# Optimization experiments

Measured on AMD Instinct MI355X. Metric: run time of the kernel, lower is better.

Reference implementation:

```python
import jax, jax.numpy as jnp
import numpy as np

N = 12288      # nodes
E = 393216     # edges (avg degree 32)
D_IN = 512
D_H = 256      # interm_dim
D_Z = 64       # latent_dim


def setup_inputs() -> dict:
    key = jax.random.key(0)
    ks = jax.random.split(key, 9)
    X = jax.random.normal(ks[0], (N, D_IN), jnp.float32)
    edge_index = jax.random.randint(ks[1], (2, E), 0, N, dtype=jnp.int64)
    # GCNConv weights (glorot-ish scaling)
    W1 = jax.random.normal(ks[2], (D_IN, D_H), jnp.float32) / np.sqrt(D_IN)
    b1 = jnp.zeros((D_H,), jnp.float32)
    Wmu = jax.random.normal(ks[3], (D_H, D_Z), jnp.float32) / np.sqrt(D_H)
    bmu = jnp.zeros((D_Z,), jnp.float32)
    Wsig = jax.random.normal(ks[4], (D_H, 1), jnp.float32) / np.sqrt(D_H)
    bsig = jnp.zeros((1,), jnp.float32)
    # reparameterization noise (torch: Normal(0,1).sample(mus.size()))
    eps = jax.random.normal(ks[5], (N, D_Z), jnp.float32)
    return {"X": X, "edge_index": edge_index, "W1": W1, "b1": b1,
            "Wmu": Wmu, "bmu": bmu, "Wsig": Wsig, "bsig": bsig, "eps": eps}


def _gcn_conv(h_in, W, b, src, dst, norm):
    # GCNConv: linear transform then symmetric-normalized aggregation with self-loops
    h = h_in @ W + b                                   # [N, F_out]
    msg = h[src] * norm[src, None]                     # gather + scale
    agg = jax.ops.segment_sum(msg, dst, num_segments=N)
    # self-loop contribution: norm_i * norm_i * h_i
    return norm[:, None] * (agg + norm[:, None] * h)


def reference(X, edge_index, W1, b1, Wmu, bmu, Wsig, bsig, eps):
    src, dst = edge_index[0], edge_index[1]
    # degree of A + I (edge weight 1, plus self loop)
    deg = jax.ops.segment_sum(jnp.ones((E,), X.dtype), dst, num_segments=N) + 1.0
    norm = jax.lax.rsqrt(deg)                          # D^{-1/2}

    # encoder
    H = jax.nn.relu(_gcn_conv(X, W1, b1, src, dst, norm))   # [N, D_H]; dropout p=0.0
    mus = _gcn_conv(H, Wmu, bmu, src, dst, norm)            # [N, D_Z]
    logsigma2s = _gcn_conv(H, Wsig, bsig, src, dst, norm)   # [N, 1]

    # reparameterize
    sigmas = jnp.exp(0.5 * logsigma2s)                      # [N, 1]
    Z = mus + sigmas * eps                                  # [N, D_Z]

    # dense decoder
    ZZt = Z @ Z.T                                           # [N, N]
    return ZZt, mus, logsigma2s
```

## Files before the change

### kernel.cpp

```cpp
#include <hip/hip_runtime.h>

#define N_NODES 12288
#define N_EDGES 393216
#define DIN 512
#define DH 256
#define DZ 64

typedef __bf16 bf16x8 __attribute__((ext_vector_type(8)));
typedef float f32x4 __attribute__((ext_vector_type(4)));
typedef unsigned short u16x8 __attribute__((ext_vector_type(8)));

static __device__ __forceinline__ unsigned short f2bf(float f) {
    unsigned int u = __float_as_uint(f);
    unsigned int r = (u + 0x7fffu + ((u >> 16) & 1u)) >> 16;
    return (unsigned short)r;
}
static __device__ __forceinline__ float bf2f(unsigned short u) {
    return __uint_as_float((unsigned int)u << 16);
}

__global__ __launch_bounds__(256) void k_prep(const float* __restrict__ X, unsigned short* __restrict__ Xb,
                                              const float* __restrict__ W1, unsigned short* __restrict__ W1T,
                                              const float* __restrict__ Wmu, unsigned short* __restrict__ WmuT,
                                              const int* __restrict__ dst, int* __restrict__ deg) {
    int b = blockIdx.x;
    if (b < 6144) {
        int i = b * 256 + threadIdx.x;
        float4 v = ((const float4*)X)[i];
        ushort4 o;
        o.x = f2bf(v.x); o.y = f2bf(v.y); o.z = f2bf(v.z); o.w = f2bf(v.w);
        ((ushort4*)Xb)[i] = o;
    } else if (b < 6656) {
        int i = (b - 6144) * 256 + threadIdx.x;
        int c = i >> 9, k = i & 511;
        W1T[i] = f2bf(W1[k * DH + c]);
    } else if (b < 6720) {
        int i = (b - 6656) * 256 + threadIdx.x;
        int c = i >> 8, k = i & 255;
        WmuT[i] = f2bf(Wmu[k * DZ + c]);
    } else {
        int e = (b - 6720) * 256 + threadIdx.x;
        atomicAdd(&deg[dst[e]], 1);
    }
}

__global__ __launch_bounds__(1024) void k_scan(const int* __restrict__ cnt, int* __restrict__ rp,
                                               float* __restrict__ norm) {
    __shared__ int sp[1024];
    int t = threadIdx.x;
    int base = t * 12;
    int loc[12];
    int s = 0;
#pragma unroll
    for (int j = 0; j < 12; ++j) {
        int c = cnt[base + j];
        norm[base + j] = rsqrtf((float)c + 1.0f);
        loc[j] = s; s += c;
    }
    sp[t] = s;
    __syncthreads();
    for (int off = 1; off < 1024; off <<= 1) {
        int v = (t >= off) ? sp[t - off] : 0;
        __syncthreads();
        sp[t] += v;
        __syncthreads();
    }
    int pre = (t == 0) ? 0 : sp[t - 1];
#pragma unroll
    for (int j = 0; j < 12; ++j) rp[base + j] = pre + loc[j];
    if (t == 1023) rp[N_NODES] = sp[1023];
}

__global__ __launch_bounds__(256) void k_scatter(const int* __restrict__ src, const int* __restrict__ dst,
                                                 const int* __restrict__ rp, int* __restrict__ cursor,
                                                 int* __restrict__ ssrc) {
    int e = blockIdx.x * 256 + threadIdx.x;
    int d = dst[e];
    int pos = atomicAdd(&cursor[d], 1);
    ssrc[rp[d] + pos] = src[e];
}

__global__ __launch_bounds__(512) void k_gemm1(const unsigned short* __restrict__ Xb,
                                               const unsigned short* __restrict__ W1T,
                                               const float* __restrict__ b1, const float* __restrict__ norm,
                                               unsigned short* __restrict__ g1) {
    int wid = threadIdx.x >> 6;
    int lane = threadIdx.x & 63;
    int ln = lane & 15, kg = lane >> 4;
    int rb = blockIdx.x * 256 + (wid >> 1) * 64;
    int cb = blockIdx.y * 128 + (wid & 1) * 64;
    f32x4 acc[4][4] = {};
    const unsigned short* xa = Xb + (size_t)(rb + ln) * DIN + kg * 8;
    const unsigned short* wb = W1T + (size_t)(cb + ln) * DIN + kg * 8;
    for (int ks = 0; ks < 16; ++ks) {
        int k0 = ks * 32;
        bf16x8 a[4], b[4];
#pragma unroll
        for (int m = 0; m < 4; ++m) a[m] = *(const bf16x8*)(xa + (size_t)m * 16 * DIN + k0);
#pragma unroll
        for (int n = 0; n < 4; ++n) b[n] = *(const bf16x8*)(wb + (size_t)n * 16 * DIN + k0);
#pragma unroll
        for (int m = 0; m < 4; ++m)
#pragma unroll
            for (int n = 0; n < 4; ++n)
                acc[m][n] = __builtin_amdgcn_mfma_f32_16x16x32_bf16(a[m], b[n], acc[m][n], 0, 0, 0);
    }
#pragma unroll
    for (int m = 0; m < 4; ++m)
#pragma unroll
        for (int r = 0; r < 4; ++r) {
            int row = rb + m * 16 + kg * 4 + r;
            float ni = norm[row];
#pragma unroll
            for (int n = 0; n < 4; ++n) {
                int col = cb + n * 16 + ln;
                g1[(size_t)row * DH + col] = f2bf(ni * (acc[m][n][r] + b1[col]));
            }
        }
}

__global__ __launch_bounds__(256) void k_agg1(const unsigned short* __restrict__ g1,
                                              const int* __restrict__ rp, const int* __restrict__ ssrc,
                                              const float* __restrict__ norm, const float* __restrict__ Wsig,
                                              unsigned short* __restrict__ G2, float* __restrict__ tvec,
                                              float* __restrict__ qv) {
    int w = threadIdx.x >> 6;
    int lane = threadIdx.x & 63;
    int half = lane >> 5, lh = lane & 31;
    int i = blockIdx.x * 4 + w;
    int beg = rp[i], end = rp[i + 1];
    int cnt = end - beg;
    int itn = (cnt + 1) >> 1;
    size_t cho = (size_t)lh * 8;
    float a8[8] = {};
    float ssum = 0.f;
#pragma unroll 2
    for (int it = 0; it < itn; ++it) {
        int e = beg + it * 2 + half;
        if (e < end) {
            int s = ssrc[e];
            u16x8 v = *(const u16x8*)(g1 + ((size_t)s << 8) + cho);
            ssum += norm[s];
#pragma unroll
            for (int j = 0; j < 8; ++j) a8[j] += bf2f(v[j]);
        }
    }
    if (half == 0) {
        u16x8 v = *(const u16x8*)(g1 + ((size_t)i << 8) + cho);
#pragma unroll
        for (int j = 0; j < 8; ++j) a8[j] += bf2f(v[j]);
    }
#pragma unroll
    for (int j = 0; j < 8; ++j) a8[j] += __shfl_xor(a8[j], 32);
    ssum += __shfl_xor(ssum, 32);
    float ni = norm[i];
    const float4 ws0 = *(const float4*)(Wsig + cho);
    const float4 ws1 = *(const float4*)(Wsig + cho + 4);
    float g[8];
#pragma unroll
    for (int j = 0; j < 8; ++j) g[j] = ni * fmaxf(ni * a8[j], 0.f);
    float qp = g[0] * ws0.x + g[1] * ws0.y + g[2] * ws0.z + g[3] * ws0.w
             + g[4] * ws1.x + g[5] * ws1.y + g[6] * ws1.z + g[7] * ws1.w;
    if (half == 0) {
        u16x8 o;
#pragma unroll
        for (int j = 0; j < 8; ++j) o[j] = f2bf(g[j]);
        *(u16x8*)(G2 + ((size_t)i << 8) + cho) = o;
    }
#pragma unroll
    for (int m = 16; m >= 1; m >>= 1) qp += __shfl_xor(qp, m);
    if (lane == 0) {
        tvec[i] = ssum + ni;
        qv[i] = qp;
    }
}

__global__ __launch_bounds__(256) void k_gemm2(const unsigned short* __restrict__ G2,
                                               const unsigned short* __restrict__ WmuT,
                                               unsigned short* __restrict__ Pb) {
    int wid = threadIdx.x >> 6;
    int lane = threadIdx.x & 63;
    int ln = lane & 15, kg = lane >> 4;
    int rb = blockIdx.x * 128 + wid * 32;
    f32x4 acc[2][4] = {};
    const unsigned short* xa = G2 + (size_t)(rb + ln) * DH + kg * 8;
    const unsigned short* wb = WmuT + (size_t)ln * DH + kg * 8;
    for (int ks = 0; ks < 8; ++ks) {
        int k0 = ks * 32;
        bf16x8 a[2], b[4];
#pragma unroll
        for (int m = 0; m < 2; ++m) a[m] = *(const bf16x8*)(xa + (size_t)m * 16 * DH + k0);
#pragma unroll
        for (int n = 0; n < 4; ++n) b[n] = *(const bf16x8*)(wb + (size_t)n * 16 * DH + k0);
#pragma unroll
        for (int m = 0; m < 2; ++m)
#pragma unroll
            for (int n = 0; n < 4; ++n)
                acc[m][n] = __builtin_amdgcn_mfma_f32_16x16x32_bf16(a[m], b[n], acc[m][n], 0, 0, 0);
    }
#pragma unroll
    for (int m = 0; m < 2; ++m)
#pragma unroll
        for (int n = 0; n < 4; ++n)
#pragma unroll
            for (int r = 0; r < 4; ++r) {
                int row = rb + m * 16 + kg * 4 + r;
                int col = n * 16 + ln;
                Pb[(size_t)row * DZ + col] = f2bf(acc[m][n][r]);
            }
}

__global__ __launch_bounds__(256) void k_agg2(const unsigned short* __restrict__ Pb,
                                              const float* __restrict__ qv,
                                              const int* __restrict__ rp, const int* __restrict__ ssrc,
                                              const float* __restrict__ norm, const float* __restrict__ tvec,
                                              const float* __restrict__ bmu, const float* __restrict__ bsig,
                                              const float* __restrict__ eps,
                                              float* __restrict__ mus_out, float* __restrict__ logs_out,
                                              unsigned short* __restrict__ Zb) {
    int w = threadIdx.x >> 6;
    int lane = threadIdx.x & 63;
    int grp = lane >> 4, li = lane & 15;
    int i = blockIdx.x * 4 + w;
    int beg = rp[i], end = rp[i + 1];
    int cnt = end - beg;
    int itn = (cnt + 3) >> 2;
    int co = li * 4;
    float a4[4] = {};
    float qa = 0.f;
#pragma unroll 2
    for (int it = 0; it < itn; ++it) {
        int e = beg + it * 4 + grp;
        if (e < end) {
            int s = ssrc[e];
            ushort4 v = *(const ushort4*)(Pb + ((size_t)s << 6) + co);
            qa += qv[s];
            a4[0] += bf2f(v.x); a4[1] += bf2f(v.y); a4[2] += bf2f(v.z); a4[3] += bf2f(v.w);
        }
    }
    if (grp == 0) {
        ushort4 v = *(const ushort4*)(Pb + ((size_t)i << 6) + co);
        qa += qv[i];
        a4[0] += bf2f(v.x); a4[1] += bf2f(v.y); a4[2] += bf2f(v.z); a4[3] += bf2f(v.w);
    }
#pragma unroll
    for (int j = 0; j < 4; ++j) {
        a4[j] += __shfl_xor(a4[j], 16);
        a4[j] += __shfl_xor(a4[j], 32);
    }
    qa += __shfl_xor(qa, 16);
    qa += __shfl_xor(qa, 32);
    float ni = norm[i], tv = tvec[i];
    float ls = ni * (qa + bsig[0] * tv);
    float sig = expf(0.5f * ls);
    if (lane == 0) logs_out[i] = ls;
    if (lane < 16) {
        const float4 bm = *(const float4*)(bmu + co);
        float4 mu;
        mu.x = ni * (a4[0] + bm.x * tv);
        mu.y = ni * (a4[1] + bm.y * tv);
        mu.z = ni * (a4[2] + bm.z * tv);
        mu.w = ni * (a4[3] + bm.w * tv);
        size_t oidx = ((size_t)i << 6) + co;
        *(float4*)(mus_out + oidx) = mu;
        const float4 ep = *(const float4*)(eps + oidx);
        ushort4 z;
        z.x = f2bf(mu.x + sig * ep.x);
        z.y = f2bf(mu.y + sig * ep.y);
        z.z = f2bf(mu.z + sig * ep.z);
        z.w = f2bf(mu.w + sig * ep.w);
        *(ushort4*)(Zb + oidx) = z;
    }
}

#define LPAD 260
__global__ __launch_bounds__(256) void k_zzt(const unsigned short* __restrict__ Zb, float* __restrict__ out) {
    __shared__ float lds[32 * LPAD];
    int w = threadIdx.x >> 6;
    int lane = threadIdx.x & 63;
    int ln = lane & 15, kg = lane >> 4;
    int rb = blockIdx.x * 64;
    int cb = blockIdx.y * 256 + w * 64;
    bf16x8 a[4][2], b[4][2];
#pragma unroll
    for (int m = 0; m < 4; ++m)
#pragma unroll
        for (int kc = 0; kc < 2; ++kc)
            a[m][kc] = *(const bf16x8*)(Zb + (size_t)(rb + m * 16 + ln) * DZ + kc * 32 + kg * 8);
#pragma unroll
    for (int n = 0; n < 4; ++n)
#pragma unroll
        for (int kc = 0; kc < 2; ++kc)
            b[n][kc] = *(const bf16x8*)(Zb + (size_t)(cb + n * 16 + ln) * DZ + kc * 32 + kg * 8);
    f32x4 acc[4][4] = {};
#pragma unroll
    for (int m = 0; m < 4; ++m)
#pragma unroll
        for (int n = 0; n < 4; ++n) {
            acc[m][n] = __builtin_amdgcn_mfma_f32_16x16x32_bf16(a[m][0], b[n][0], acc[m][n], 0, 0, 0);
            acc[m][n] = __builtin_amdgcn_mfma_f32_16x16x32_bf16(a[m][1], b[n][1], acc[m][n], 0, 0, 0);
        }
    int c4 = (threadIdx.x & 63) * 4;
    int rw = threadIdx.x >> 6;
    size_t colbase = (size_t)blockIdx.y * 256 + c4;
#pragma unroll
    for (int p = 0; p < 2; ++p) {
        if (p) __syncthreads();
#pragma unroll
        for (int mm = 0; mm < 2; ++mm) {
            int m = p * 2 + mm;
#pragma unroll
            for (int n = 0; n < 4; ++n)
#pragma unroll
                for (int r = 0; r < 4; ++r)
                    lds[(mm * 16 + kg * 4 + r) * LPAD + w * 64 + n * 16 + ln] = acc[m][n][r];
        }
        __syncthreads();
#pragma unroll
        for (int it = 0; it < 8; ++it) {
            int rl = it * 4 + rw;
            f32x4 v = *(const f32x4*)&lds[rl * LPAD + c4];
            __builtin_nontemporal_store(v, (f32x4*)(out + (size_t)(rb + p * 32 + rl) * N_NODES + colbase));
        }
    }
}

extern "C" void kernel_launch(void* const* d_in, const int* in_sizes, int n_in,
                              void* d_out, int out_size, void* d_ws, size_t ws_size,
                              hipStream_t stream) {
    const float* X = (const float*)d_in[0];
    const int* edge = (const int*)d_in[1];
    const float* W1 = (const float*)d_in[2];
    const float* b1 = (const float*)d_in[3];
    const float* Wmu = (const float*)d_in[4];
    const float* bmu = (const float*)d_in[5];
    const float* Wsig = (const float*)d_in[6];
    const float* bsig = (const float*)d_in[7];
    const float* eps = (const float*)d_in[8];

    const int* esrc = edge;
    const int* edst = edge + N_EDGES;

    char* w = (char*)d_ws;
    int* deg = (int*)w;            w += (size_t)N_NODES * 4;
    int* cursor = (int*)w;         w += (size_t)N_NODES * 4;
    float* norm = (float*)w;       w += (size_t)N_NODES * 4;
    float* tvec = (float*)w;       w += (size_t)N_NODES * 4;
    float* qv = (float*)w;         w += (size_t)N_NODES * 4;
    int* rowptr = (int*)w;         w += (size_t)(N_NODES + 64) * 4;
    int* ssrc = (int*)w;           w += (size_t)N_EDGES * 4;
    unsigned short* Xb = (unsigned short*)w;   w += (size_t)N_NODES * DIN * 2;
    unsigned short* W1T = (unsigned short*)w;  w += (size_t)DIN * DH * 2;
    unsigned short* WmuT = (unsigned short*)w; w += (size_t)DH * DZ * 2;
    unsigned short* g1 = (unsigned short*)w;   w += (size_t)N_NODES * DH * 2;
    unsigned short* G2 = (unsigned short*)w;   w += (size_t)N_NODES * DH * 2;
    unsigned short* Pb = (unsigned short*)w;   w += (size_t)N_NODES * DZ * 2;
    unsigned short* Zb = (unsigned short*)w;   w += (size_t)N_NODES * DZ * 2;

    float* out_zzt = (float*)d_out;
    float* out_mus = out_zzt + (size_t)N_NODES * N_NODES;
    float* out_logs = out_mus + (size_t)N_NODES * DZ;

    hipMemsetAsync(d_ws, 0, (size_t)N_NODES * 8, stream);
    k_prep<<<8256, 256, 0, stream>>>(X, Xb, W1, W1T, Wmu, WmuT, edst, deg);
    k_scan<<<1, 1024, 0, stream>>>(deg, rowptr, norm);
    k_scatter<<<N_EDGES / 256, 256, 0, stream>>>(esrc, edst, rowptr, cursor, ssrc);
    k_gemm1<<<dim3(N_NODES / 256, 2), 512, 0, stream>>>(Xb, W1T, b1, norm, g1);
    k_agg1<<<N_NODES / 4, 256, 0, stream>>>(g1, rowptr, ssrc, norm, Wsig, G2, tvec, qv);
    k_gemm2<<<N_NODES / 128, 256, 0, stream>>>(G2, WmuT, Pb);
    k_agg2<<<N_NODES / 4, 256, 0, stream>>>(Pb, qv, rowptr, ssrc, norm, tvec, bmu, bsig, eps,
                                            out_mus, out_logs, Zb);
    k_zzt<<<dim3(N_NODES / 64, N_NODES / 256), 256, 0, stream>>>(Zb, out_zzt);
}
```

Baseline: 278.4 us.

## Split hidden features into halves, XCD-aware aggregation, fold Wsig into gemm2

Stores the hidden activations as two 128-column halves and maps aggregation blocks so that each group of XCDs gathers only one half. The goal is a smaller gathered working set per L2. The Wsig projection moves out of agg1 and becomes an extra MFMA column tile in gemm2 (WmuT80), and cursor zeroing moves into the scan kernel so the memset shrinks. The ZZt kernel also swaps its grid axes and drops nontemporal stores. The trade-offs are twice as many agg1 blocks with duplicated index and rowptr reads, a different write-back pattern for the large ZZt output, and reliance on the assumed round-robin block-to-XCD mapping.

```diff
diff --git a/kernel.cpp b/kernel.cpp
--- a/kernel.cpp
+++ b/kernel.cpp
@@ -5,10 +5,11 @@
 #define DIN 512
 #define DH 256
 #define DZ 64
+#define HALF 128
 
 typedef __bf16 bf16x8 __attribute__((ext_vector_type(8)));
 typedef float f32x4 __attribute__((ext_vector_type(4)));
-typedef unsigned short u16x8 __attribute__((ext_vector_type(8)));
+typedef unsigned short u16x4 __attribute__((ext_vector_type(4)));
 
 static __device__ __forceinline__ unsigned short f2bf(float f) {
     unsigned int u = __float_as_uint(f);
@@ -21,7 +22,8 @@
 
 __global__ __launch_bounds__(256) void k_prep(const float* __restrict__ X, unsigned short* __restrict__ Xb,
                                               const float* __restrict__ W1, unsigned short* __restrict__ W1T,
-                                              const float* __restrict__ Wmu, unsigned short* __restrict__ WmuT,
+                                              const float* __restrict__ Wmu, const float* __restrict__ Wsig,
+                                              unsigned short* __restrict__ WmuT80,
                                               const int* __restrict__ dst, int* __restrict__ deg) {
     int b = blockIdx.x;
     if (b < 6144) {
@@ -34,18 +36,19 @@
         int i = (b - 6144) * 256 + threadIdx.x;
         int c = i >> 9, k = i & 511;
         W1T[i] = f2bf(W1[k * DH + c]);
-    } else if (b < 6720) {
+    } else if (b < 6736) {
         int i = (b - 6656) * 256 + threadIdx.x;
         int c = i >> 8, k = i & 255;
-        WmuT[i] = f2bf(Wmu[k * DZ + c]);
+        float v = (c < 64) ? Wmu[k * DZ + c] : ((c == 64) ? Wsig[k] : 0.f);
+        WmuT80[i] = f2bf(v);
     } else {
-        int e = (b - 6720) * 256 + threadIdx.x;
+        int e = (b - 6736) * 256 + threadIdx.x;
         atomicAdd(&deg[dst[e]], 1);
     }
 }
 
 __global__ __launch_bounds__(1024) void k_scan(const int* __restrict__ cnt, int* __restrict__ rp,
-                                               float* __restrict__ norm) {
+                                               float* __restrict__ norm, int* __restrict__ cursor) {
     __shared__ int sp[1024];
     int t = threadIdx.x;
     int base = t * 12;
@@ -55,6 +58,7 @@
     for (int j = 0; j < 12; ++j) {
         int c = cnt[base + j];
         norm[base + j] = rsqrtf((float)c + 1.0f);
+        cursor[base + j] = 0;
         loc[j] = s; s += c;
     }
     sp[t] = s;
@@ -83,7 +87,7 @@
 __global__ __launch_bounds__(512) void k_gemm1(const unsigned short* __restrict__ Xb,
                                                const unsigned short* __restrict__ W1T,
                                                const float* __restrict__ b1, const float* __restrict__ norm,
-                                               unsigned short* __restrict__ g1) {
+                                               unsigned short* __restrict__ g1a, unsigned short* __restrict__ g1b) {
     int wid = threadIdx.x >> 6;
     int lane = threadIdx.x & 63;
     int ln = lane & 15, kg = lane >> 4;
@@ -105,6 +109,8 @@
             for (int n = 0; n < 4; ++n)
                 acc[m][n] = __builtin_amdgcn_mfma_f32_16x16x32_bf16(a[m], b[n], acc[m][n], 0, 0, 0);
     }
+    unsigned short* gout = (cb < 128) ? g1a : g1b;
+    int cbh = cb & 64;
 #pragma unroll
     for (int m = 0; m < 4; ++m)
 #pragma unroll
@@ -114,100 +120,97 @@
 #pragma unroll
             for (int n = 0; n < 4; ++n) {
                 int col = cb + n * 16 + ln;
-                g1[(size_t)row * DH + col] = f2bf(ni * (acc[m][n][r] + b1[col]));
+                gout[(size_t)row * HALF + cbh + n * 16 + ln] = f2bf(ni * (acc[m][n][r] + b1[col]));
             }
         }
 }
 
-__global__ __launch_bounds__(256) void k_agg1(const unsigned short* __restrict__ g1,
+__global__ __launch_bounds__(256) void k_agg1(const unsigned short* __restrict__ g1a,
+                                              const unsigned short* __restrict__ g1b,
                                               const int* __restrict__ rp, const int* __restrict__ ssrc,
-                                              const float* __restrict__ norm, const float* __restrict__ Wsig,
-                                              unsigned short* __restrict__ G2, float* __restrict__ tvec,
-                                              float* __restrict__ qv) {
+                                              const float* __restrict__ norm,
+                                              unsigned short* __restrict__ G2a, unsigned short* __restrict__ G2b,
+                                              float* __restrict__ tvec) {
+    int b = blockIdx.x;
+    int xcdp = b & 7;
+    int pass = xcdp >> 2;
+    int sub = xcdp & 3;
+    int idx = (b >> 3) * 4 + sub;
     int w = threadIdx.x >> 6;
     int lane = threadIdx.x & 63;
     int half = lane >> 5, lh = lane & 31;
-    int i = blockIdx.x * 4 + w;
+    int i = idx * 4 + w;
     int beg = rp[i], end = rp[i + 1];
     int cnt = end - beg;
     int itn = (cnt + 1) >> 1;
-    size_t cho = (size_t)lh * 8;
-    float a8[8] = {};
+    int cho = lh * 4;
+    const unsigned short* gsrc = pass ? g1b : g1a;
+    float a4[4] = {};
     float ssum = 0.f;
 #pragma unroll 2
     for (int it = 0; it < itn; ++it) {
         int e = beg + it * 2 + half;
         if (e < end) {
-            int s = ssrc[e];
-            u16x8 v = *(const u16x8*)(g1 + ((size_t)s << 8) + cho);
-            ssum += norm[s];
-#pragma unroll
-            for (int j = 0; j < 8; ++j) a8[j] += bf2f(v[j]);
+            int s = __builtin_nontemporal_load(ssrc + e);
+            ushort4 v = *(const ushort4*)(gsrc + (size_t)s * HALF + cho);
+            if (pass == 0) ssum += norm[s];
+            a4[0] += bf2f(v.x); a4[1] += bf2f(v.y); a4[2] += bf2f(v.z); a4[3] += bf2f(v.w);
         }
     }
     if (half == 0) {
-        u16x8 v = *(const u16x8*)(g1 + ((size_t)i << 8) + cho);
-#pragma unroll
-        for (int j = 0; j < 8; ++j) a8[j] += bf2f(v[j]);
-    }
-#pragma unroll
-    for (int j = 0; j < 8; ++j) a8[j] += __shfl_xor(a8[j], 32);
+        ushort4 v = *(const ushort4*)(gsrc + (size_t)i * HALF + cho);
+        a4[0] += bf2f(v.x); a4[1] += bf2f(v.y); a4[2] += bf2f(v.z); a4[3] += bf2f(v.w);
+    }
+#pragma unroll
+    for (int j = 0; j < 4; ++j) a4[j] += __shfl_xor(a4[j], 32);
     ssum += __shfl_xor(ssum, 32);
     float ni = norm[i];
-    const float4 ws0 = *(const float4*)(Wsig + cho);
-    const float4 ws1 = *(const float4*)(Wsig + cho + 4);
-    float g[8];
-#pragma unroll
-    for (int j = 0; j < 8; ++j) g[j] = ni * fmaxf(ni * a8[j], 0.f);
-    float qp = g[0] * ws0.x + g[1] * ws0.y + g[2] * ws0.z + g[3] * ws0.w
-             + g[4] * ws1.x + g[5] * ws1.y + g[6] * ws1.z + g[7] * ws1.w;
     if (half == 0) {
-        u16x8 o;
-#pragma unroll
-        for (int j = 0; j < 8; ++j) o[j] = f2bf(g[j]);
-        *(u16x8*)(G2 + ((size_t)i << 8) + cho) = o;
-    }
-#pragma unroll
-    for (int m = 16; m >= 1; m >>= 1) qp += __shfl_xor(qp, m);
-    if (lane == 0) {
-        tvec[i] = ssum + ni;
-        qv[i] = qp;
-    }
-}
-
-__global__ __launch_bounds__(256) void k_gemm2(const unsigned short* __restrict__ G2,
-                                               const unsigned short* __restrict__ WmuT,
-                                               unsigned short* __restrict__ Pb) {
+        u16x4 o;
+        o[0] = f2bf(ni * fmaxf(ni * a4[0], 0.f));
+        o[1] = f2bf(ni * fmaxf(ni * a4[1], 0.f));
+        o[2] = f2bf(ni * fmaxf(ni * a4[2], 0.f));
+        o[3] = f2bf(ni * fmaxf(ni * a4[3], 0.f));
+        unsigned short* gdst = pass ? G2b : G2a;
+        __builtin_nontemporal_store(o, (u16x4*)(gdst + (size_t)i * HALF + cho));
+    }
+    if (pass == 0 && lane == 0) tvec[i] = ssum + ni;
+}
+
+__global__ __launch_bounds__(256) void k_gemm2(const unsigned short* __restrict__ G2a,
+                                               const unsigned short* __restrict__ G2b,
+                                               const unsigned short* __restrict__ WmuT80,
+                                               unsigned short* __restrict__ Pb, float* __restrict__ qv) {
     int wid = threadIdx.x >> 6;
     int lane = threadIdx.x & 63;
     int ln = lane & 15, kg = lane >> 4;
     int rb = blockIdx.x * 128 + wid * 32;
-    f32x4 acc[2][4] = {};
-    const unsigned short* xa = G2 + (size_t)(rb + ln) * DH + kg * 8;
-    const unsigned short* wb = WmuT + (size_t)ln * DH + kg * 8;
+    f32x4 acc[2][5] = {};
+    const unsigned short* wb = WmuT80 + (size_t)ln * 256 + kg * 8;
     for (int ks = 0; ks < 8; ++ks) {
         int k0 = ks * 32;
-        bf16x8 a[2], b[4];
-#pragma unroll
-        for (int m = 0; m < 2; ++m) a[m] = *(const bf16x8*)(xa + (size_t)m * 16 * DH + k0);
-#pragma unroll
-        for (int n = 0; n < 4; ++n) b[n] = *(const bf16x8*)(wb + (size_t)n * 16 * DH + k0);
+        const unsigned short* xsrc = (ks < 4) ? (G2a + kg * 8 + ks * 32) : (G2b + kg * 8 + (ks - 4) * 32);
+        bf16x8 a[2], b[5];
+#pragma unroll
+        for (int m = 0; m < 2; ++m) a[m] = *(const bf16x8*)(xsrc + (size_t)(rb + m * 16 + ln) * HALF);
+#pragma unroll
+        for (int n = 0; n < 5; ++n) b[n] = *(const bf16x8*)(wb + (size_t)n * 16 * 256 + k0);
 #pragma unroll
         for (int m = 0; m < 2; ++m)
 #pragma unroll
+            for (int n = 0; n < 5; ++n)
+                acc[m][n] = __builtin_amdgcn_mfma_f32_16x16x32_bf16(a[m], b[n], acc[m][n], 0, 0, 0);
+    }
+#pragma unroll
+    for (int m = 0; m < 2; ++m)
+#pragma unroll
+        for (int r = 0; r < 4; ++r) {
+            int row = rb + m * 16 + kg * 4 + r;
+#pragma unroll
             for (int n = 0; n < 4; ++n)
-                acc[m][n] = __builtin_amdgcn_mfma_f32_16x16x32_bf16(a[m], b[n], acc[m][n], 0, 0, 0);
-    }
-#pragma unroll
-    for (int m = 0; m < 2; ++m)
-#pragma unroll
-        for (int n = 0; n < 4; ++n)
-#pragma unroll
-            for (int r = 0; r < 4; ++r) {
-                int row = rb + m * 16 + kg * 4 + r;
-                int col = n * 16 + ln;
-                Pb[(size_t)row * DZ + col] = f2bf(acc[m][n][r]);
-            }
+                Pb[(size_t)row * DZ + n * 16 + ln] = f2bf(acc[m][n][r]);
+            if (ln == 0) qv[row] = acc[m][4][r];
+        }
 }
 
 __global__ __launch_bounds__(256) void k_agg2(const unsigned short* __restrict__ Pb,
@@ -279,8 +282,8 @@
     int w = threadIdx.x >> 6;
     int lane = threadIdx.x & 63;
     int ln = lane & 15, kg = lane >> 4;
-    int rb = blockIdx.x * 64;
-    int cb = blockIdx.y * 256 + w * 64;
+    int rb = blockIdx.y * 64;
+    int cb = blockIdx.x * 256 + w * 64;
     bf16x8 a[4][2], b[4][2];
 #pragma unroll
     for (int m = 0; m < 4; ++m)
@@ -302,7 +305,7 @@
         }
     int c4 = (threadIdx.x & 63) * 4;
     int rw = threadIdx.x >> 6;
-    size_t colbase = (size_t)blockIdx.y * 256 + c4;
+    size_t colbase = (size_t)blockIdx.x * 256 + c4;
 #pragma unroll
     for (int p = 0; p < 2; ++p) {
         if (p) __syncthreads();
@@ -320,7 +323,7 @@
         for (int it = 0; it < 8; ++it) {
             int rl = it * 4 + rw;
             f32x4 v = *(const f32x4*)&lds[rl * LPAD + c4];
-            __builtin_nontemporal_store(v, (f32x4*)(out + (size_t)(rb + p * 32 + rl) * N_NODES + colbase));
+            *(f32x4*)(out + (size_t)(rb + p * 32 + rl) * N_NODES + colbase) = v;
         }
     }
 }
@@ -349,26 +352,28 @@
     float* qv = (float*)w;         w += (size_t)N_NODES * 4;
     int* rowptr = (int*)w;         w += (size_t)(N_NODES + 64) * 4;
     int* ssrc = (int*)w;           w += (size_t)N_EDGES * 4;
-    unsigned short* Xb = (unsigned short*)w;   w += (size_t)N_NODES * DIN * 2;
-    unsigned short* W1T = (unsigned short*)w;  w += (size_t)DIN * DH * 2;
-    unsigned short* WmuT = (unsigned short*)w; w += (size_t)DH * DZ * 2;
-    unsigned short* g1 = (unsigned short*)w;   w += (size_t)N_NODES * DH * 2;
-    unsigned short* G2 = (unsigned short*)w;   w += (size_t)N_NODES * DH * 2;
-    unsigned short* Pb = (unsigned short*)w;   w += (size_t)N_NODES * DZ * 2;
-    unsigned short* Zb = (unsigned short*)w;   w += (size_t)N_NODES * DZ * 2;
+    unsigned short* Xb = (unsigned short*)w;    w += (size_t)N_NODES * DIN * 2;
+    unsigned short* W1T = (unsigned short*)w;   w += (size_t)DIN * DH * 2;
+    unsigned short* WmuT80 = (unsigned short*)w; w += (size_t)80 * 256 * 2;
+    unsigned short* g1a = (unsigned short*)w;   w += (size_t)N_NODES * HALF * 2;
+    unsigned short* g1b = (unsigned short*)w;   w += (size_t)N_NODES * HALF * 2;
+    unsigned short* G2a = (unsigned short*)w;   w += (size_t)N_NODES * HALF * 2;
+    unsigned short* G2b = (unsigned short*)w;   w += (size_t)N_NODES * HALF * 2;
+    unsigned short* Pb = (unsigned short*)w;    w += (size_t)N_NODES * DZ * 2;
+    unsigned short* Zb = (unsigned short*)w;    w += (size_t)N_NODES * DZ * 2;
 
     float* out_zzt = (float*)d_out;
     float* out_mus = out_zzt + (size_t)N_NODES * N_NODES;
     float* out_logs = out_mus + (size_t)N_NODES * DZ;
 
-    hipMemsetAsync(d_ws, 0, (size_t)N_NODES * 8, stream);
-    k_prep<<<8256, 256, 0, stream>>>(X, Xb, W1, W1T, Wmu, WmuT, edst, deg);
-    k_scan<<<1, 1024, 0, stream>>>(deg, rowptr, norm);
+    (void)hipMemsetAsync(deg, 0, (size_t)N_NODES * 4, stream);
+    k_prep<<<8272, 256, 0, stream>>>(X, Xb, W1, W1T, Wmu, Wsig, WmuT80, edst, deg);
+    k_scan<<<1, 1024, 0, stream>>>(deg, rowptr, norm, cursor);
     k_scatter<<<N_EDGES / 256, 256, 0, stream>>>(esrc, edst, rowptr, cursor, ssrc);
-    k_gemm1<<<dim3(N_NODES / 256, 2), 512, 0, stream>>>(Xb, W1T, b1, norm, g1);
-    k_agg1<<<N_NODES / 4, 256, 0, stream>>>(g1, rowptr, ssrc, norm, Wsig, G2, tvec, qv);
-    k_gemm2<<<N_NODES / 128, 256, 0, stream>>>(G2, WmuT, Pb);
+    k_gemm1<<<dim3(N_NODES / 256, 2), 512, 0, stream>>>(Xb, W1T, b1, norm, g1a, g1b);
+    k_agg1<<<N_NODES / 2, 256, 0, stream>>>(g1a, g1b, rowptr, ssrc, norm, G2a, G2b, tvec);
+    k_gemm2<<<N_NODES / 128, 256, 0, stream>>>(G2a, G2b, WmuT80, Pb, qv);
     k_agg2<<<N_NODES / 4, 256, 0, stream>>>(Pb, qv, rowptr, ssrc, norm, tvec, bmu, bsig, eps,
                                             out_mus, out_logs, Zb);
-    k_zzt<<<dim3(N_NODES / 64, N_NODES / 256), 256, 0, stream>>>(Zb, out_zzt);
-}
+    k_zzt<<<dim3(N_NODES / 256, N_NODES / 64), 256, 0, stream>>>(Zb, out_zzt);
+}
```

Result: slower. 285.3 us (+2.5%).

## Fuse all pre-decoder stages into one persistent kernel with grid barriers

Applied to the files above, without the earlier changes.

Replaces the seven separate launches (prep, scan, scatter, gemm1, agg1, gemm2, agg2) with one persistent kernel of 512 blocks. The stages are separated by software grid barriers built from atomic counters. This removes per-launch overhead and the tail gaps between the many small kernels. The costs are less parallelism in each stage: gemm1 uses smaller tiles with fewer waves, and the scan now runs on a single block. The design also depends on all 512 blocks being resident at once, otherwise the barriers deadlock.

```diff
diff --git a/kernel.cpp b/kernel.cpp
--- a/kernel.cpp
+++ b/kernel.cpp
@@ -5,6 +5,8 @@
 #define DIN 512
 #define DH 256
 #define DZ 64
+#define NB 512
+#define NT 256
 
 typedef __bf16 bf16x8 __attribute__((ext_vector_type(8)));
 typedef float f32x4 __attribute__((ext_vector_type(4)));
@@ -19,257 +21,256 @@
     return __uint_as_float((unsigned int)u << 16);
 }
 
-__global__ __launch_bounds__(256) void k_prep(const float* __restrict__ X, unsigned short* __restrict__ Xb,
-                                              const float* __restrict__ W1, unsigned short* __restrict__ W1T,
-                                              const float* __restrict__ Wmu, unsigned short* __restrict__ WmuT,
-                                              const int* __restrict__ dst, int* __restrict__ deg) {
-    int b = blockIdx.x;
-    if (b < 6144) {
-        int i = b * 256 + threadIdx.x;
+static __device__ __forceinline__ void gridbar(int* bar, int p) {
+    __syncthreads();
+    if (threadIdx.x == 0) {
+        __threadfence();
+        __hip_atomic_fetch_add(&bar[p], 1, __ATOMIC_RELEASE, __HIP_MEMORY_SCOPE_AGENT);
+        while (__hip_atomic_load(&bar[p], __ATOMIC_ACQUIRE, __HIP_MEMORY_SCOPE_AGENT) < NB)
+            __builtin_amdgcn_s_sleep(2);
+        __threadfence();
+    }
+    __syncthreads();
+}
+
+__global__ __launch_bounds__(256, 2) void k_mega(
+    const float* __restrict__ X, const int* __restrict__ esrc, const int* __restrict__ edst,
+    const float* __restrict__ W1, const float* __restrict__ Wmu, const float* __restrict__ Wsig,
+    const float* __restrict__ b1, const float* __restrict__ bmu, const float* __restrict__ bsig,
+    const float* __restrict__ eps,
+    int* __restrict__ bar, int* __restrict__ deg, int* __restrict__ cursor,
+    float* __restrict__ norm, float* __restrict__ tvec, float* __restrict__ qv,
+    int* __restrict__ rp, int* __restrict__ ssrc,
+    unsigned short* __restrict__ Xb, unsigned short* __restrict__ W1T, unsigned short* __restrict__ WmuT,
+    unsigned short* __restrict__ g1, unsigned short* __restrict__ G2, unsigned short* __restrict__ Pb,
+    float* __restrict__ mus_out, float* __restrict__ logs_out, unsigned short* __restrict__ Zb) {
+
+    __shared__ int sp[256];
+    const int tid = threadIdx.x;
+    const int bid = blockIdx.x;
+    const int gtid = bid * NT + tid;
+    const int w = tid >> 6, lane = tid & 63;
+    const int gw = bid * 4 + w;
+
+    for (int i = gtid; i < N_NODES * DIN / 4; i += NB * NT) {
         float4 v = ((const float4*)X)[i];
         ushort4 o;
         o.x = f2bf(v.x); o.y = f2bf(v.y); o.z = f2bf(v.z); o.w = f2bf(v.w);
         ((ushort4*)Xb)[i] = o;
-    } else if (b < 6656) {
-        int i = (b - 6144) * 256 + threadIdx.x;
-        int c = i >> 9, k = i & 511;
-        W1T[i] = f2bf(W1[k * DH + c]);
-    } else if (b < 6720) {
-        int i = (b - 6656) * 256 + threadIdx.x;
-        int c = i >> 8, k = i & 255;
-        WmuT[i] = f2bf(Wmu[k * DZ + c]);
-    } else {
-        int e = (b - 6720) * 256 + threadIdx.x;
-        atomicAdd(&deg[dst[e]], 1);
-    }
-}
-
-__global__ __launch_bounds__(1024) void k_scan(const int* __restrict__ cnt, int* __restrict__ rp,
-                                               float* __restrict__ norm) {
-    __shared__ int sp[1024];
-    int t = threadIdx.x;
-    int base = t * 12;
-    int loc[12];
-    int s = 0;
-#pragma unroll
-    for (int j = 0; j < 12; ++j) {
-        int c = cnt[base + j];
-        norm[base + j] = rsqrtf((float)c + 1.0f);
-        loc[j] = s; s += c;
-    }
-    sp[t] = s;
-    __syncthreads();
-    for (int off = 1; off < 1024; off <<= 1) {
-        int v = (t >= off) ? sp[t - off] : 0;
+    }
+    {
+        int c = gtid >> 9, k = gtid & 511;
+        W1T[gtid] = f2bf(W1[k * DH + c]);
+    }
+    if (gtid < DH * DZ) {
+        int c = gtid >> 8, k = gtid & 255;
+        WmuT[gtid] = f2bf(Wmu[k * DZ + c]);
+    }
+    for (int e = gtid; e < N_EDGES; e += NB * NT)
+        atomicAdd(&deg[edst[e]], 1);
+
+    gridbar(bar, 0);
+
+    if (bid == 0) {
+        int base = tid * 48;
+        int s = 0;
+        for (int j = 0; j < 48; ++j) s += deg[base + j];
+        sp[tid] = s;
         __syncthreads();
-        sp[t] += v;
-        __syncthreads();
-    }
-    int pre = (t == 0) ? 0 : sp[t - 1];
-#pragma unroll
-    for (int j = 0; j < 12; ++j) rp[base + j] = pre + loc[j];
-    if (t == 1023) rp[N_NODES] = sp[1023];
-}
-
-__global__ __launch_bounds__(256) void k_scatter(const int* __restrict__ src, const int* __restrict__ dst,
-                                                 const int* __restrict__ rp, int* __restrict__ cursor,
-                                                 int* __restrict__ ssrc) {
-    int e = blockIdx.x * 256 + threadIdx.x;
-    int d = dst[e];
-    int pos = atomicAdd(&cursor[d], 1);
-    ssrc[rp[d] + pos] = src[e];
-}
-
-__global__ __launch_bounds__(512) void k_gemm1(const unsigned short* __restrict__ Xb,
-                                               const unsigned short* __restrict__ W1T,
-                                               const float* __restrict__ b1, const float* __restrict__ norm,
-                                               unsigned short* __restrict__ g1) {
-    int wid = threadIdx.x >> 6;
-    int lane = threadIdx.x & 63;
-    int ln = lane & 15, kg = lane >> 4;
-    int rb = blockIdx.x * 256 + (wid >> 1) * 64;
-    int cb = blockIdx.y * 128 + (wid & 1) * 64;
-    f32x4 acc[4][4] = {};
-    const unsigned short* xa = Xb + (size_t)(rb + ln) * DIN + kg * 8;
-    const unsigned short* wb = W1T + (size_t)(cb + ln) * DIN + kg * 8;
-    for (int ks = 0; ks < 16; ++ks) {
-        int k0 = ks * 32;
-        bf16x8 a[4], b[4];
-#pragma unroll
-        for (int m = 0; m < 4; ++m) a[m] = *(const bf16x8*)(xa + (size_t)m * 16 * DIN + k0);
-#pragma unroll
-        for (int n = 0; n < 4; ++n) b[n] = *(const bf16x8*)(wb + (size_t)n * 16 * DIN + k0);
-#pragma unroll
-        for (int m = 0; m < 4; ++m)
-#pragma unroll
-            for (int n = 0; n < 4; ++n)
-                acc[m][n] = __builtin_amdgcn_mfma_f32_16x16x32_bf16(a[m], b[n], acc[m][n], 0, 0, 0);
-    }
-#pragma unroll
-    for (int m = 0; m < 4; ++m)
-#pragma unroll
-        for (int r = 0; r < 4; ++r) {
-            int row = rb + m * 16 + kg * 4 + r;
-            float ni = norm[row];
-#pragma unroll
-            for (int n = 0; n < 4; ++n) {
-                int col = cb + n * 16 + ln;
-                g1[(size_t)row * DH + col] = f2bf(ni * (acc[m][n][r] + b1[col]));
-            }
-        }
-}
-
-__global__ __launch_bounds__(256) void k_agg1(const unsigned short* __restrict__ g1,
-                                              const int* __restrict__ rp, const int* __restrict__ ssrc,
-                                              const float* __restrict__ norm, const float* __restrict__ Wsig,
-                                              unsigned short* __restrict__ G2, float* __restrict__ tvec,
-                                              float* __restrict__ qv) {
-    int w = threadIdx.x >> 6;
-    int lane = threadIdx.x & 63;
-    int half = lane >> 5, lh = lane & 31;
-    int i = blockIdx.x * 4 + w;
-    int beg = rp[i], end = rp[i + 1];
-    int cnt = end - beg;
-    int itn = (cnt + 1) >> 1;
-    size_t cho = (size_t)lh * 8;
-    float a8[8] = {};
-    float ssum = 0.f;
+        for (int off = 1; off < 256; off <<= 1) {
+            int v = (tid >= off) ? sp[tid - off] : 0;
+            __syncthreads();
+            sp[tid] += v;
+            __syncthreads();
+        }
+        int run = (tid == 0) ? 0 : sp[tid - 1];
+        for (int j = 0; j < 48; ++j) { rp[base + j] = run; run += deg[base + j]; }
+        if (tid == 255) rp[N_NODES] = run;
+    }
+    if (gtid < N_NODES) {
+        norm[gtid] = rsqrtf((float)deg[gtid] + 1.0f);
+        cursor[gtid] = 0;
+    }
+    gridbar(bar, 1);
+
+    for (int e = gtid; e < N_EDGES; e += NB * NT) {
+        int d = edst[e];
+        int pos = atomicAdd(&cursor[d], 1);
+        ssrc[rp[d] + pos] = esrc[e];
+    }
+    gridbar(bar, 2);
+
+    {
+        int ln = lane & 15, kg = lane >> 4;
+        for (int j = bid; j < 384; j += NB) {
+            int rb = (j >> 2) * 128 + w * 32;
+            int cb = (j & 3) * 64;
+            f32x4 acc[2][4] = {};
+            const unsigned short* xa = Xb + (size_t)(rb + ln) * DIN + kg * 8;
+            const unsigned short* wb = W1T + (size_t)(cb + ln) * DIN + kg * 8;
+            for (int ks = 0; ks < 16; ++ks) {
+                int k0 = ks * 32;
+                bf16x8 a[2], b[4];
+#pragma unroll
+                for (int m = 0; m < 2; ++m) a[m] = *(const bf16x8*)(xa + (size_t)m * 16 * DIN + k0);
+#pragma unroll
+                for (int n = 0; n < 4; ++n) b[n] = *(const bf16x8*)(wb + (size_t)n * 16 * DIN + k0);
+#pragma unroll
+                for (int m = 0; m < 2; ++m)
+#pragma unroll
+                    for (int n = 0; n < 4; ++n)
+                        acc[m][n] = __builtin_amdgcn_mfma_f32_16x16x32_bf16(a[m], b[n], acc[m][n], 0, 0, 0);
+            }
+#pragma unroll
+            for (int m = 0; m < 2; ++m)
+#pragma unroll
+                for (int r = 0; r < 4; ++r) {
+                    int row = rb + m * 16 + kg * 4 + r;
+                    float ni = norm[row];
+#pragma unroll
+                    for (int n = 0; n < 4; ++n) {
+                        int col = cb + n * 16 + ln;
+                        g1[(size_t)row * DH + col] = f2bf(ni * (acc[m][n][r] + b1[col]));
+                    }
+                }
+        }
+    }
+    gridbar(bar, 3);
+
+    {
+        int half = lane >> 5, lh = lane & 31;
+        size_t cho = (size_t)lh * 8;
+        for (int i = gw; i < N_NODES; i += 2048) {
+            int beg = rp[i], end = rp[i + 1];
+            int itn = (end - beg + 1) >> 1;
+            float a8[8] = {};
+            float ssum = 0.f;
 #pragma unroll 2
-    for (int it = 0; it < itn; ++it) {
-        int e = beg + it * 2 + half;
-        if (e < end) {
-            int s = ssrc[e];
-            u16x8 v = *(const u16x8*)(g1 + ((size_t)s << 8) + cho);
-            ssum += norm[s];
-#pragma unroll
-            for (int j = 0; j < 8; ++j) a8[j] += bf2f(v[j]);
-        }
-    }
-    if (half == 0) {
-        u16x8 v = *(const u16x8*)(g1 + ((size_t)i << 8) + cho);
-#pragma unroll
-        for (int j = 0; j < 8; ++j) a8[j] += bf2f(v[j]);
-    }
-#pragma unroll
-    for (int j = 0; j < 8; ++j) a8[j] += __shfl_xor(a8[j], 32);
-    ssum += __shfl_xor(ssum, 32);
-    float ni = norm[i];
-    const float4 ws0 = *(const float4*)(Wsig + cho);
-    const float4 ws1 = *(const float4*)(Wsig + cho + 4);
-    float g[8];
-#pragma unroll
-    for (int j = 0; j < 8; ++j) g[j] = ni * fmaxf(ni * a8[j], 0.f);
-    float qp = g[0] * ws0.x + g[1] * ws0.y + g[2] * ws0.z + g[3] * ws0.w
-             + g[4] * ws1.x + g[5] * ws1.y + g[6] * ws1.z + g[7] * ws1.w;
-    if (half == 0) {
-        u16x8 o;
-#pragma unroll
-        for (int j = 0; j < 8; ++j) o[j] = f2bf(g[j]);
-        *(u16x8*)(G2 + ((size_t)i << 8) + cho) = o;
-    }
-#pragma unroll
-    for (int m = 16; m >= 1; m >>= 1) qp += __shfl_xor(qp, m);
-    if (lane == 0) {
-        tvec[i] = ssum + ni;
-        qv[i] = qp;
-    }
-}
-
-__global__ __launch_bounds__(256) void k_gemm2(const unsigned short* __restrict__ G2,
-                                               const unsigned short* __restrict__ WmuT,
-                                               unsigned short* __restrict__ Pb) {
-    int wid = threadIdx.x >> 6;
-    int lane = threadIdx.x & 63;
-    int ln = lane & 15, kg = lane >> 4;
-    int rb = blockIdx.x * 128 + wid * 32;
-    f32x4 acc[2][4] = {};
-    const unsigned short* xa = G2 + (size_t)(rb + ln) * DH + kg * 8;
-    const unsigned short* wb = WmuT + (size_t)ln * DH + kg * 8;
-    for (int ks = 0; ks < 8; ++ks) {
-        int k0 = ks * 32;
-        bf16x8 a[2], b[4];
-#pragma unroll
-        for (int m = 0; m < 2; ++m) a[m] = *(const bf16x8*)(xa + (size_t)m * 16 * DH + k0);
-#pragma unroll
-        for (int n = 0; n < 4; ++n) b[n] = *(const bf16x8*)(wb + (size_t)n * 16 * DH + k0);
-#pragma unroll
-        for (int m = 0; m < 2; ++m)
-#pragma unroll
-            for (int n = 0; n < 4; ++n)
-                acc[m][n] = __builtin_amdgcn_mfma_f32_16x16x32_bf16(a[m], b[n], acc[m][n], 0, 0, 0);
-    }
-#pragma unroll
-    for (int m = 0; m < 2; ++m)
-#pragma unroll
-        for (int n = 0; n < 4; ++n)
-#pragma unroll
-            for (int r = 0; r < 4; ++r) {
-                int row = rb + m * 16 + kg * 4 + r;
-                int col = n * 16 + ln;
-                Pb[(size_t)row * DZ + col] = f2bf(acc[m][n][r]);
-            }
-}
-
-__global__ __launch_bounds__(256) void k_agg2(const unsigned short* __restrict__ Pb,
-                                              const float* __restrict__ qv,
-                                              const int* __restrict__ rp, const int* __restrict__ ssrc,
-                                              const float* __restrict__ norm, const float* __restrict__ tvec,
-                                              const float* __restrict__ bmu, const float* __restrict__ bsig,
-                                              const float* __restrict__ eps,
-                                              float* __restrict__ mus_out, float* __restrict__ logs_out,
-                                              unsigned short* __restrict__ Zb) {
-    int w = threadIdx.x >> 6;
-    int lane = threadIdx.x & 63;
-    int grp = lane >> 4, li = lane & 15;
-    int i = blockIdx.x * 4 + w;
-    int beg = rp[i], end = rp[i + 1];
-    int cnt = end - beg;
-    int itn = (cnt + 3) >> 2;
-    int co = li * 4;
-    float a4[4] = {};
-    float qa = 0.f;
+            for (int it = 0; it < itn; ++it) {
+                int e = beg + it * 2 + half;
+                if (e < end) {
+                    int s = ssrc[e];
+                    u16x8 v = *(const u16x8*)(g1 + ((size_t)s << 8) + cho);
+                    ssum += norm[s];
+#pragma unroll
+                    for (int j = 0; j < 8; ++j) a8[j] += bf2f(v[j]);
+                }
+            }
+            if (half == 0) {
+                u16x8 v = *(const u16x8*)(g1 + ((size_t)i << 8) + cho);
+#pragma unroll
+                for (int j = 0; j < 8; ++j) a8[j] += bf2f(v[j]);
+            }
+#pragma unroll
+            for (int j = 0; j < 8; ++j) a8[j] += __shfl_xor(a8[j], 32);
+            ssum += __shfl_xor(ssum, 32);
+            float ni = norm[i];
+            const float4 ws0 = *(const float4*)(Wsig + cho);
+            const float4 ws1 = *(const float4*)(Wsig + cho + 4);
+            float g[8];
+#pragma unroll
+            for (int j = 0; j < 8; ++j) g[j] = ni * fmaxf(ni * a8[j], 0.f);
+            float qp = g[0] * ws0.x + g[1] * ws0.y + g[2] * ws0.z + g[3] * ws0.w
+                     + g[4] * ws1.x + g[5] * ws1.y + g[6] * ws1.z + g[7] * ws1.w;
+            if (half == 0) {
+                u16x8 o;
+#pragma unroll
+                for (int j = 0; j < 8; ++j) o[j] = f2bf(g[j]);
+                *(u16x8*)(G2 + ((size_t)i << 8) + cho) = o;
+            }
+#pragma unroll
+            for (int m = 16; m >= 1; m >>= 1) qp += __shfl_xor(qp, m);
+            if (lane == 0) {
+                tvec[i] = ssum + ni;
+                qv[i] = qp;
+            }
+        }
+    }
+    gridbar(bar, 4);
+
+    {
+        int ln = lane & 15, kg = lane >> 4;
+        for (int jw = gw; jw < 384; jw += 2048) {
+            int rb = jw * 32;
+            f32x4 acc[2][4] = {};
+            const unsigned short* xa = G2 + (size_t)(rb + ln) * DH + kg * 8;
+            const unsigned short* wb = WmuT + (size_t)ln * DH + kg * 8;
+            for (int ks = 0; ks < 8; ++ks) {
+                int k0 = ks * 32;
+                bf16x8 a[2], b[4];
+#pragma unroll
+                for (int m = 0; m < 2; ++m) a[m] = *(const bf16x8*)(xa + (size_t)m * 16 * DH + k0);
+#pragma unroll
+                for (int n = 0; n < 4; ++n) b[n] = *(const bf16x8*)(wb + (size_t)n * 16 * DH + k0);
+#pragma unroll
+                for (int m = 0; m < 2; ++m)
+#pragma unroll
+                    for (int n = 0; n < 4; ++n)
+                        acc[m][n] = __builtin_amdgcn_mfma_f32_16x16x32_bf16(a[m], b[n], acc[m][n], 0, 0, 0);
+            }
+#pragma unroll
+            for (int m = 0; m < 2; ++m)
+#pragma unroll
+                for (int n = 0; n < 4; ++n)
+#pragma unroll
+                    for (int r = 0; r < 4; ++r)
+                        Pb[(size_t)(rb + m * 16 + kg * 4 + r) * DZ + n * 16 + ln] = f2bf(acc[m][n][r]);
+        }
+    }
+    gridbar(bar, 5);
+
+    {
+        int grp = lane >> 4, li = lane & 15;
+        int co = li * 4;
+        for (int i = gw; i < N_NODES; i += 2048) {
+            int beg = rp[i], end = rp[i + 1];
+            int itn = (end - beg + 3) >> 2;
+            float a4[4] = {};
+            float qa = 0.f;
 #pragma unroll 2
-    for (int it = 0; it < itn; ++it) {
-        int e = beg + it * 4 + grp;
-        if (e < end) {
-            int s = ssrc[e];
-            ushort4 v = *(const ushort4*)(Pb + ((size_t)s << 6) + co);
-            qa += qv[s];
-            a4[0] += bf2f(v.x); a4[1] += bf2f(v.y); a4[2] += bf2f(v.z); a4[3] += bf2f(v.w);
-        }
-    }
-    if (grp == 0) {
-        ushort4 v = *(const ushort4*)(Pb + ((size_t)i << 6) + co);
-        qa += qv[i];
-        a4[0] += bf2f(v.x); a4[1] += bf2f(v.y); a4[2] += bf2f(v.z); a4[3] += bf2f(v.w);
-    }
-#pragma unroll
-    for (int j = 0; j < 4; ++j) {
-        a4[j] += __shfl_xor(a4[j], 16);
-        a4[j] += __shfl_xor(a4[j], 32);
-    }
-    qa += __shfl_xor(qa, 16);
-    qa += __shfl_xor(qa, 32);
-    float ni = norm[i], tv = tvec[i];
-    float ls = ni * (qa + bsig[0] * tv);
-    float sig = expf(0.5f * ls);
-    if (lane == 0) logs_out[i] = ls;
-    if (lane < 16) {
-        const float4 bm = *(const float4*)(bmu + co);
-        float4 mu;
-        mu.x = ni * (a4[0] + bm.x * tv);
-        mu.y = ni * (a4[1] + bm.y * tv);
-        mu.z = ni * (a4[2] + bm.z * tv);
-        mu.w = ni * (a4[3] + bm.w * tv);
-        size_t oidx = ((size_t)i << 6) + co;
-        *(float4*)(mus_out + oidx) = mu;
-        const float4 ep = *(const float4*)(eps + oidx);
-        ushort4 z;
-        z.x = f2bf(mu.x + sig * ep.x);
-        z.y = f2bf(mu.y + sig * ep.y);
-        z.z = f2bf(mu.z + sig * ep.z);
-        z.w = f2bf(mu.w + sig * ep.w);
-        *(ushort4*)(Zb + oidx) = z;
+            for (int it = 0; it < itn; ++it) {
+                int e = beg + it * 4 + grp;
+                if (e < end) {
+                    int s = ssrc[e];
+                    ushort4 v = *(const ushort4*)(Pb + ((size_t)s << 6) + co);
+                    qa += qv[s];
+                    a4[0] += bf2f(v.x); a4[1] += bf2f(v.y); a4[2] += bf2f(v.z); a4[3] += bf2f(v.w);
+                }
+            }
+            if (grp == 0) {
+                ushort4 v = *(const ushort4*)(Pb + ((size_t)i << 6) + co);
+                qa += qv[i];
+                a4[0] += bf2f(v.x); a4[1] += bf2f(v.y); a4[2] += bf2f(v.z); a4[3] += bf2f(v.w);
+            }
+#pragma unroll
+            for (int j = 0; j < 4; ++j) {
+                a4[j] += __shfl_xor(a4[j], 16);
+                a4[j] += __shfl_xor(a4[j], 32);
+            }
+            qa += __shfl_xor(qa, 16);
+            qa += __shfl_xor(qa, 32);
+            float ni = norm[i], tv = tvec[i];
+            float ls = ni * (qa + bsig[0] * tv);
+            float sig = expf(0.5f * ls);
+            if (lane == 0) logs_out[i] = ls;
+            if (lane < 16) {
+                const float4 bm = *(const float4*)(bmu + co);
+                float4 mu;
+                mu.x = ni * (a4[0] + bm.x * tv);
+                mu.y = ni * (a4[1] + bm.y * tv);
+                mu.z = ni * (a4[2] + bm.z * tv);
+                mu.w = ni * (a4[3] + bm.w * tv);
+                size_t oidx = ((size_t)i << 6) + co;
+                *(float4*)(mus_out + oidx) = mu;
+                const float4 ep = *(const float4*)(eps + oidx);
+                ushort4 z;
+                z.x = f2bf(mu.x + sig * ep.x);
+                z.y = f2bf(mu.y + sig * ep.y);
+                z.z = f2bf(mu.z + sig * ep.z);
+                z.w = f2bf(mu.w + sig * ep.w);
+                *(ushort4*)(Zb + oidx) = z;
+            }
+        }
     }
 }
 
@@ -342,6 +343,7 @@
     const int* edst = edge + N_EDGES;
 
     char* w = (char*)d_ws;
+    int* bar = (int*)w;            w += 64;
     int* deg = (int*)w;            w += (size_t)N_NODES * 4;
     int* cursor = (int*)w;         w += (size_t)N_NODES * 4;
     float* norm = (float*)w;       w += (size_t)N_NODES * 4;
@@ -361,14 +363,10 @@
     float* out_mus = out_zzt + (size_t)N_NODES * N_NODES;
     float* out_logs = out_mus + (size_t)N_NODES * DZ;
 
-    hipMemsetAsync(d_ws, 0, (size_t)N_NODES * 8, stream);
-    k_prep<<<8256, 256, 0, stream>>>(X, Xb, W1, W1T, Wmu, WmuT, edst, deg);
-    k_scan<<<1, 1024, 0, stream>>>(deg, rowptr, norm);
-    k_scatter<<<N_EDGES / 256, 256, 0, stream>>>(esrc, edst, rowptr, cursor, ssrc);
-    k_gemm1<<<dim3(N_NODES / 256, 2), 512, 0, stream>>>(Xb, W1T, b1, norm, g1);
-    k_agg1<<<N_NODES / 4, 256, 0, stream>>>(g1, rowptr, ssrc, norm, Wsig, G2, tvec, qv);
-    k_gemm2<<<N_NODES / 128, 256, 0, stream>>>(G2, WmuT, Pb);
-    k_agg2<<<N_NODES / 4, 256, 0, stream>>>(Pb, qv, rowptr, ssrc, norm, tvec, bmu, bsig, eps,
-                                            out_mus, out_logs, Zb);
+    (void)hipMemsetAsync(d_ws, 0, 64 + (size_t)N_NODES * 4, stream);
+    k_mega<<<NB, NT, 0, stream>>>(X, esrc, edst, W1, Wmu, Wsig, b1, bmu, bsig, eps,
+                                  bar, deg, cursor, norm, tvec, qv, rowptr, ssrc,
+                                  Xb, W1T, WmuT, g1, G2, Pb,
+                                  out_mus, out_logs, Zb);
     k_zzt<<<dim3(N_NODES / 64, N_NODES / 256), 256, 0, stream>>>(Zb, out_zzt);
 }
```

Measured after the change: 867.9 us. 212% more time.
